# Kernel tuning notes

Hardware: AMD Instinct MI355X
Metric: run time of the kernel (lower is better)

The kernel has to match this reference:

```python
import jax, jax.numpy as jnp
import numpy as np


def setup_inputs() -> dict:
    key = jax.random.key(0)
    ks = jax.random.split(key, 8)
    B, N, A, H = 2, 2048, 256, 8
    KD = A // H  # key_dim per head = 32
    VD = A // H  # value_dim per head = 32
    return {
        "q_data": jax.random.normal(ks[0], (B, N, A), dtype=jnp.float32),
        "bias": jax.random.normal(ks[1], (B, N), dtype=jnp.float32),
        "nonbatched_bias": jax.random.normal(ks[2], (H, N, N), dtype=jnp.float32),
        "query_w": jax.random.normal(ks[3], (A, H, KD), dtype=jnp.float32) * 0.05,
        "query_b": jax.random.normal(ks[4], (1, H, KD), dtype=jnp.float32) * 0.05,
        "key_w": jax.random.normal(ks[5], (A, H, KD), dtype=jnp.float32) * 0.05,
        "value_w": jax.random.normal(ks[6], (A, H, VD), dtype=jnp.float32) * 0.05,
        "gating_w": jax.random.normal(ks[7], (A, H, VD), dtype=jnp.float32) * 0.05,
    }


def reference(q_data, bias, nonbatched_bias, query_w, query_b, key_w, value_w, gating_w):
    # q_data: [b, n, a]; bias: [b, n_k]; nonbatched_bias: [h, n_q, n_k]
    key_dim = query_w.shape[-1]
    scale = key_dim ** (-0.5)
    # projections (fused QKV in the original kernel)
    q = (jnp.einsum("bqa,ahc->bqhc", q_data, query_w) + query_b) * scale  # [b,q,h,c]
    k = jnp.einsum("bka,ahc->bkhc", q_data, key_w)                        # [b,k,h,c]
    v = jnp.einsum("bka,ahv->bkhv", q_data, value_w)                      # [b,k,h,v]
    # attention logits + batched bias (over keys) + shared nonbatched bias
    logits = jnp.einsum("bqhc,bkhc->bhqk", q, k)
    logits = logits + bias[:, None, None, :] + nonbatched_bias[None]
    weights = jax.nn.softmax(logits, axis=-1)                             # [b,h,q,k]
    weighted = jnp.einsum("bhqk,bkhv->bqhv", weights, v)                  # [b,q,h,v]
    # sigmoid gating branch fused after value projection
    gate = jax.nn.sigmoid(jnp.einsum("bqa,ahv->bqhv", q_data, gating_w))
    return weighted * gate                                                # [b,q,h,v]
```

## Files before the change

### kernel.cpp

```cpp
#include <hip/hip_runtime.h>
#include <stdint.h>

#define NTOK 2048
#define SCALE 0.17677669529663687f

typedef short s16x8 __attribute__((ext_vector_type(8)));
typedef unsigned short u16x8 __attribute__((ext_vector_type(8)));
typedef float f32x4 __attribute__((ext_vector_type(4)));

__device__ __forceinline__ unsigned short f2bf(float f) {
  unsigned int u = __builtin_bit_cast(unsigned int, f);
  u += 0x7fffu + ((u >> 16) & 1u);
  return (unsigned short)(u >> 16);
}

__global__ __launch_bounds__(256) void prep_weights_k(
    const float* __restrict__ qw, const float* __restrict__ kw,
    const float* __restrict__ vw, const float* __restrict__ gw,
    unsigned short* __restrict__ Wt) {
  __shared__ float tile[64][68];
  const int p = blockIdx.z;
  const int a0 = blockIdx.x * 64;
  const int n0 = blockIdx.y * 64;
  const float* src = (p == 0) ? qw : (p == 1) ? kw : (p == 2) ? vw : gw;
  const int tx = threadIdx.x & 15;
  const int ty = threadIdx.x >> 4;
#pragma unroll
  for (int kk = 0; kk < 4; kk++) {
    int ar = ty + kk * 16;
    float4 v = *reinterpret_cast<const float4*>(src + (a0 + ar) * 256 + n0 + tx * 4);
    tile[ar][tx * 4 + 0] = v.x; tile[ar][tx * 4 + 1] = v.y;
    tile[ar][tx * 4 + 2] = v.z; tile[ar][tx * 4 + 3] = v.w;
  }
  __syncthreads();
  unsigned short* dst = Wt + p * 65536;
#pragma unroll
  for (int kk = 0; kk < 4; kk++) {
    int nr = ty + kk * 16;
    ushort4 o;
    o.x = f2bf(tile[tx * 4 + 0][nr]);
    o.y = f2bf(tile[tx * 4 + 1][nr]);
    o.z = f2bf(tile[tx * 4 + 2][nr]);
    o.w = f2bf(tile[tx * 4 + 3][nr]);
    *reinterpret_cast<ushort4*>(dst + (n0 + nr) * 256 + a0 + tx * 4) = o;
  }
}

__global__ __launch_bounds__(256) void proj_k(
    const float* __restrict__ x, const unsigned short* __restrict__ Wt,
    const float* __restrict__ query_b,
    unsigned short* __restrict__ Qg, unsigned short* __restrict__ Kg,
    unsigned short* __restrict__ Vt, float* __restrict__ gate) {
  const int w = threadIdx.x >> 6;
  const int lane = threadIdx.x & 63;
  const int l15 = lane & 15;
  const int quad = lane >> 4;
  const int p = blockIdx.y >> 1;
  const int half = blockIdx.y & 1;
  const int rbase = blockIdx.x * 128 + w * 32;
  const unsigned short* wp = Wt + p * 65536;

  f32x4 acc[2][8];
#pragma unroll
  for (int rt = 0; rt < 2; rt++)
#pragma unroll
    for (int ct = 0; ct < 8; ct++) acc[rt][ct] = (f32x4){0.f, 0.f, 0.f, 0.f};

  for (int ks = 0; ks < 8; ks++) {
    const int kb = ks * 32;
    s16x8 af[2];
#pragma unroll
    for (int rt = 0; rt < 2; rt++) {
      const float* xr = x + (rbase + rt * 16 + l15) * 256 + kb + quad * 8;
      float4 f0 = *reinterpret_cast<const float4*>(xr);
      float4 f1 = *reinterpret_cast<const float4*>(xr + 4);
      u16x8 t;
      t[0] = f2bf(f0.x); t[1] = f2bf(f0.y); t[2] = f2bf(f0.z); t[3] = f2bf(f0.w);
      t[4] = f2bf(f1.x); t[5] = f2bf(f1.y); t[6] = f2bf(f1.z); t[7] = f2bf(f1.w);
      af[rt] = __builtin_bit_cast(s16x8, t);
    }
#pragma unroll
    for (int ct = 0; ct < 8; ct++) {
      uint4 bv = *reinterpret_cast<const uint4*>(
          wp + (half * 128 + ct * 16 + l15) * 256 + kb + quad * 8);
      s16x8 bfr = __builtin_bit_cast(s16x8, bv);
#pragma unroll
      for (int rt = 0; rt < 2; rt++)
        acc[rt][ct] = __builtin_amdgcn_mfma_f32_16x16x32_bf16(af[rt], bfr, acc[rt][ct], 0, 0, 0);
    }
  }

#pragma unroll
  for (int ct = 0; ct < 8; ct++) {
    const int cgl = half * 128 + ct * 16 + l15;
    const int h = cgl >> 5, c = cgl & 31;
#pragma unroll
    for (int rt = 0; rt < 2; rt++) {
      const int n0r = rbase + rt * 16 + quad * 4;
      const int bidx = n0r >> 11;
      const int nl0 = n0r & 2047;
      if (p == 0) {
        const float qb = query_b[cgl];
#pragma unroll
        for (int i = 0; i < 4; i++) {
          float v = (acc[rt][ct][i] + qb) * SCALE;
          Qg[(size_t)((bidx * 8 + h) * 2048 + nl0 + i) * 32 + c] = f2bf(v);
        }
      } else if (p == 1) {
#pragma unroll
        for (int i = 0; i < 4; i++)
          Kg[(size_t)((bidx * 8 + h) * 2048 + nl0 + i) * 32 + c] = f2bf(acc[rt][ct][i]);
      } else if (p == 2) {
        ushort4 o;
        o.x = f2bf(acc[rt][ct][0]); o.y = f2bf(acc[rt][ct][1]);
        o.z = f2bf(acc[rt][ct][2]); o.w = f2bf(acc[rt][ct][3]);
        *reinterpret_cast<ushort4*>(Vt + (size_t)((bidx * 8 + h) * 32 + c) * 2048 + nl0) = o;
      } else {
#pragma unroll
        for (int i = 0; i < 4; i++) {
          float s = 1.f / (1.f + __expf(-acc[rt][ct][i]));
          gate[(size_t)(bidx * 2048 + nl0 + i) * 256 + cgl] = s;
        }
      }
    }
  }
}

#define PST 136
__global__ __launch_bounds__(128, 1) void attn_k(
    const unsigned short* __restrict__ Qg, const unsigned short* __restrict__ Kg,
    const unsigned short* __restrict__ Vt, const float* __restrict__ bias,
    const float* __restrict__ nb, const float* __restrict__ gate,
    float* __restrict__ out) {
  __shared__ unsigned short Ps[2 * 16 * PST];
  const int w = threadIdx.x >> 6;
  const int lane = threadIdx.x & 63;
  const int l15 = lane & 15;
  const int quad = lane >> 4;
  const int h = blockIdx.y;
  const int qbase = blockIdx.x * 32 + w * 16;
  const int qr0 = qbase + quad * 4;
  const float* nbp = nb + (size_t)h * 2048 * 2048;
  unsigned short* Pw = Ps + w * 16 * PST;

  s16x8 aq[2];
#pragma unroll
  for (int bt = 0; bt < 2; bt++)
    aq[bt] = __builtin_bit_cast(s16x8, *reinterpret_cast<const uint4*>(
        Qg + (size_t)((bt * 8 + h) * 2048 + qbase + l15) * 32 + quad * 8));

  float psum[2][4];
  f32x4 o[2][2];
#pragma unroll
  for (int bt = 0; bt < 2; bt++)
#pragma unroll
    for (int i = 0; i < 4; i++) psum[bt][i] = 0.f;
#pragma unroll
  for (int bt = 0; bt < 2; bt++)
#pragma unroll
    for (int vt = 0; vt < 2; vt++) o[bt][vt] = (f32x4){0.f, 0.f, 0.f, 0.f};

  float nbuf[2][32];
#pragma unroll
  for (int ct = 0; ct < 8; ct++)
#pragma unroll
    for (int i = 0; i < 4; i++)
      nbuf[0][ct * 4 + i] = nbp[(size_t)(qr0 + i) * 2048 + ct * 16 + l15];

#pragma unroll 2
  for (int kt = 0; kt < 16; kt++) {
    const int kb = kt * 128;
    const int cur = kt & 1, nxt = cur ^ 1;

#pragma unroll
    for (int bt = 0; bt < 2; bt++) {
      const unsigned short* Kp = Kg + (size_t)(bt * 8 + h) * 2048 * 32;
      const unsigned short* Vp = Vt + (size_t)(bt * 8 + h) * 32 * 2048;

      s16x8 bk[8];
#pragma unroll
      for (int ct = 0; ct < 8; ct++)
        bk[ct] = __builtin_bit_cast(s16x8, *reinterpret_cast<const uint4*>(
            Kp + (size_t)(kb + ct * 16 + l15) * 32 + quad * 8));
      s16x8 vv[8];
#pragma unroll
      for (int kc = 0; kc < 4; kc++)
#pragma unroll
        for (int vt = 0; vt < 2; vt++)
          vv[kc * 2 + vt] = __builtin_bit_cast(s16x8, *reinterpret_cast<const uint4*>(
              Vp + (size_t)(vt * 16 + l15) * 2048 + kb + kc * 32 + quad * 8));
      float bbv[8];
#pragma unroll
      for (int ct = 0; ct < 8; ct++)
        bbv[ct] = bias[bt * 2048 + kb + ct * 16 + l15] - 20.f;

      if (bt == 1 && kt < 15) {
        const int kb2 = kb + 128;
#pragma unroll
        for (int ct = 0; ct < 8; ct++)
#pragma unroll
          for (int i = 0; i < 4; i++)
            nbuf[nxt][ct * 4 + i] = nbp[(size_t)(qr0 + i) * 2048 + kb2 + ct * 16 + l15];
      }

      f32x4 s[8];
#pragma unroll
      for (int ct = 0; ct < 8; ct++)
        s[ct] = __builtin_amdgcn_mfma_f32_16x16x32_bf16(
            aq[bt], bk[ct], (f32x4){0.f, 0.f, 0.f, 0.f}, 0, 0, 0);

#pragma unroll
      for (int ct = 0; ct < 8; ct++)
#pragma unroll
        for (int i = 0; i < 4; i++) {
          float pv = __expf(s[ct][i] + bbv[ct] + nbuf[cur][ct * 4 + i]);
          Pw[(quad * 4 + i) * PST + ct * 16 + l15] = f2bf(pv);
          psum[bt][i] += pv;
        }

#pragma unroll
      for (int kc = 0; kc < 4; kc++) {
        s16x8 ap = __builtin_bit_cast(s16x8, *reinterpret_cast<const uint4*>(
            &Pw[l15 * PST + kc * 32 + quad * 8]));
#pragma unroll
        for (int vt = 0; vt < 2; vt++)
          o[bt][vt] = __builtin_amdgcn_mfma_f32_16x16x32_bf16(ap, vv[kc * 2 + vt],
                                                              o[bt][vt], 0, 0, 0);
      }
    }
  }

#pragma unroll
  for (int bt = 0; bt < 2; bt++)
#pragma unroll
    for (int i = 0; i < 4; i++) {
      float l = psum[bt][i];
      l += __shfl_xor(l, 1);
      l += __shfl_xor(l, 2);
      l += __shfl_xor(l, 4);
      l += __shfl_xor(l, 8);
      const float inv = 1.f / l;
      const int q = qr0 + i;
#pragma unroll
      for (int vt = 0; vt < 2; vt++) {
        const int v = vt * 16 + l15;
        const size_t oidx = (size_t)(bt * 2048 + q) * 256 + h * 32 + v;
        out[oidx] = o[bt][vt][i] * inv * gate[oidx];
      }
    }
}

extern "C" void kernel_launch(void* const* d_in, const int* in_sizes, int n_in,
                              void* d_out, int out_size, void* d_ws, size_t ws_size,
                              hipStream_t stream) {
  const float* q_data = (const float*)d_in[0];
  const float* bias = (const float*)d_in[1];
  const float* nbb = (const float*)d_in[2];
  const float* qw = (const float*)d_in[3];
  const float* qb = (const float*)d_in[4];
  const float* kw = (const float*)d_in[5];
  const float* vw = (const float*)d_in[6];
  const float* gw = (const float*)d_in[7];
  float* out = (float*)d_out;

  char* ws = (char*)d_ws;
  unsigned short* Wt = (unsigned short*)(ws + 0);
  unsigned short* Qg = (unsigned short*)(ws + 524288);
  unsigned short* Kg = (unsigned short*)(ws + 2621440);
  unsigned short* Vt = (unsigned short*)(ws + 4718592);
  float* gate = (float*)(ws + 6815744);

  prep_weights_k<<<dim3(4, 4, 4), 256, 0, stream>>>(qw, kw, vw, gw, Wt);
  proj_k<<<dim3(32, 8), 256, 0, stream>>>(q_data, Wt, qb, Qg, Kg, Vt, gate);
  attn_k<<<dim3(64, 8), 128, 0, stream>>>(Qg, Kg, Vt, bias, nbb, gate, out);
}
```

Baseline: 273.5 us.

## Split attention key range across four blocks with atomic accumulation

Measured after the change: 424.3 us. +55.1%, slower.

```diff
diff --git a/kernel.cpp b/kernel.cpp
--- a/kernel.cpp
+++ b/kernel.cpp
@@ -127,17 +127,18 @@
 }
 
 #define PST 136
-__global__ __launch_bounds__(128, 1) void attn_k(
+__global__ __launch_bounds__(128, 3) void attn_k(
     const unsigned short* __restrict__ Qg, const unsigned short* __restrict__ Kg,
     const unsigned short* __restrict__ Vt, const float* __restrict__ bias,
-    const float* __restrict__ nb, const float* __restrict__ gate,
-    float* __restrict__ out) {
+    const float* __restrict__ nb, float* __restrict__ out,
+    float* __restrict__ psum_g) {
   __shared__ unsigned short Ps[2 * 16 * PST];
   const int w = threadIdx.x >> 6;
   const int lane = threadIdx.x & 63;
   const int l15 = lane & 15;
   const int quad = lane >> 4;
   const int h = blockIdx.y;
+  const int seg = blockIdx.z;
   const int qbase = blockIdx.x * 32 + w * 16;
   const int qr0 = qbase + quad * 4;
   const float* nbp = nb + (size_t)h * 2048 * 2048;
@@ -160,17 +161,18 @@
 #pragma unroll
     for (int vt = 0; vt < 2; vt++) o[bt][vt] = (f32x4){0.f, 0.f, 0.f, 0.f};
 
+  const int kb0 = seg * 512;
   float nbuf[2][32];
 #pragma unroll
   for (int ct = 0; ct < 8; ct++)
 #pragma unroll
     for (int i = 0; i < 4; i++)
-      nbuf[0][ct * 4 + i] = nbp[(size_t)(qr0 + i) * 2048 + ct * 16 + l15];
+      nbuf[0][ct * 4 + i] = nbp[(size_t)(qr0 + i) * 2048 + kb0 + ct * 16 + l15];
 
 #pragma unroll 2
-  for (int kt = 0; kt < 16; kt++) {
-    const int kb = kt * 128;
-    const int cur = kt & 1, nxt = cur ^ 1;
+  for (int t = 0; t < 4; t++) {
+    const int kb = kb0 + t * 128;
+    const int cur = t & 1, nxt = cur ^ 1;
 
 #pragma unroll
     for (int bt = 0; bt < 2; bt++) {
@@ -194,7 +196,7 @@
       for (int ct = 0; ct < 8; ct++)
         bbv[ct] = bias[bt * 2048 + kb + ct * 16 + l15] - 20.f;
 
-      if (bt == 1 && kt < 15) {
+      if (bt == 1 && t < 3) {
         const int kb2 = kb + 128;
 #pragma unroll
         for (int ct = 0; ct < 8; ct++)
@@ -239,15 +241,31 @@
       l += __shfl_xor(l, 2);
       l += __shfl_xor(l, 4);
       l += __shfl_xor(l, 8);
-      const float inv = 1.f / l;
       const int q = qr0 + i;
+      if (l15 == 0) atomicAdd(&psum_g[(size_t)(bt * 8 + h) * 2048 + q], l);
 #pragma unroll
       for (int vt = 0; vt < 2; vt++) {
         const int v = vt * 16 + l15;
-        const size_t oidx = (size_t)(bt * 2048 + q) * 256 + h * 32 + v;
-        out[oidx] = o[bt][vt][i] * inv * gate[oidx];
-      }
-    }
+        atomicAdd(&out[(size_t)(bt * 2048 + q) * 256 + h * 32 + v], o[bt][vt][i]);
+      }
+    }
+}
+
+__global__ __launch_bounds__(256) void finish_k(
+    float* __restrict__ out, const float* __restrict__ gate,
+    const float* __restrict__ psum_g) {
+  const int i4 = blockIdx.x * 256 + threadIdx.x;
+  const int flat = i4 * 4;
+  const int b = flat >> 19;
+  const int rem = flat & 524287;
+  const int q = rem >> 8;
+  const int c = rem & 255;
+  const int h = c >> 5;
+  const float inv = 1.f / psum_g[(size_t)(b * 8 + h) * 2048 + q];
+  float4 o = reinterpret_cast<float4*>(out)[i4];
+  float4 g = reinterpret_cast<const float4*>(gate)[i4];
+  o.x *= inv * g.x; o.y *= inv * g.y; o.z *= inv * g.z; o.w *= inv * g.w;
+  reinterpret_cast<float4*>(out)[i4] = o;
 }
 
 extern "C" void kernel_launch(void* const* d_in, const int* in_sizes, int n_in,
@@ -269,8 +287,12 @@
   unsigned short* Kg = (unsigned short*)(ws + 2621440);
   unsigned short* Vt = (unsigned short*)(ws + 4718592);
   float* gate = (float*)(ws + 6815744);
-
+  float* psum_g = (float*)(ws + 11010048);
+
+  hipMemsetAsync(out, 0, (size_t)out_size * sizeof(float), stream);
+  hipMemsetAsync(psum_g, 0, 2 * 8 * 2048 * sizeof(float), stream);
   prep_weights_k<<<dim3(4, 4, 4), 256, 0, stream>>>(qw, kw, vw, gw, Wt);
   proj_k<<<dim3(32, 8), 256, 0, stream>>>(q_data, Wt, qb, Qg, Kg, Vt, gate);
-  attn_k<<<dim3(64, 8), 128, 0, stream>>>(Qg, Kg, Vt, bias, nbb, gate, out);
-}
+  attn_k<<<dim3(64, 8, 4), 128, 0, stream>>>(Qg, Kg, Vt, bias, nbb, out, psum_g);
+  finish_k<<<dim3(1024), 256, 0, stream>>>(out, gate, psum_g);
+}
```
